# Kernel optimization log

Hardware: AMD Instinct MI355X
Metric: run time of the kernel (lower is better)

The kernel has to match this reference:

```python
import jax, jax.numpy as jnp
import numpy as np

EPS = 1e-7  # K.epsilon()
ITERATIONS = 5


def squash(v):
    # Faithful to the source: epsilon added elementwise to the vector first.
    v = v + EPS
    norm = jnp.sum(v * v, axis=-1, keepdims=True)  # squared norm
    scale = norm / (1.0 + norm) / jnp.sqrt(norm)
    return scale * v


def setup_inputs() -> dict:
    key = jax.random.key(0)
    k1, k2 = jax.random.split(key)
    B, I, D = 32, 2048, 16   # batch, input capsules, input capsule dim
    J, C = 64, 32            # output capsules, output capsule dim
    x = jax.random.normal(k1, (B, I, D), dtype=jnp.float32)
    # glorot_uniform for w_ij (fan_in = D, fan_out = C on the contracting dims)
    limit = np.sqrt(6.0 / (D + C)).astype(np.float32)
    w_ij = jax.random.uniform(k2, (J, I, C, D), dtype=jnp.float32,
                              minval=-limit, maxval=limit)
    return {"x": x, "w_ij": w_ij}


def reference(x, w_ij):
    # x: [B, I, D], w_ij: [J, I, C, D]
    # prediction vectors u_hat: [B, J, I, C]
    u_hat = jnp.einsum('bid,jicd->bjic', x, w_ij)
    B, J, I, C = u_hat.shape
    b_ij = jnp.zeros((B, J, I), dtype=u_hat.dtype)
    v_j = None
    for it in range(ITERATIONS):
        c_ij = jax.nn.softmax(b_ij, axis=1)          # softmax over output caps J
        s_j = jnp.einsum('bji,bjic->bjc', c_ij, u_hat)
        v_j = squash(s_j)                            # [B, J, C]
        if it < ITERATIONS - 1:
            b_ij = b_ij + jnp.einsum('bjc,bjic->bji', v_j, u_hat)
    return v_j
```

## Files before the change

kernel.cpp:

```cpp
#include <hip/hip_runtime.h>
#include <hip/hip_bf16.h>

#define B_ 32
#define I_ 2048
#define D_ 16
#define J_ 64
#define C_ 32

typedef float f32x16 __attribute__((ext_vector_type(16)));
typedef float f32x4a __attribute__((ext_vector_type(4)));
typedef short bf16x8 __attribute__((ext_vector_type(8)));

union BF8 { unsigned u[4]; bf16x8 v; };

__device__ __forceinline__ float bf2f(unsigned short u) {
  unsigned v = ((unsigned)u) << 16;
  float f;
  __builtin_memcpy(&f, &v, 4);
  return f;
}
__device__ __forceinline__ unsigned short f2bf(float f) {
  unsigned u;
  __builtin_memcpy(&u, &f, 4);
  u += 0x7FFFu + ((u >> 16) & 1u);
  return (unsigned short)(u >> 16);
}
__device__ __forceinline__ unsigned pk2(float lo, float hi) {
  return (unsigned)f2bf(lo) | ((unsigned)f2bf(hi) << 16);
}

__global__ __launch_bounds__(256) void prep_w(const float* __restrict__ w,
                                              unsigned short* __restrict__ w_bf,
                                              unsigned short* __restrict__ w2) {
  __shared__ float tr[16 * 33];
  const int tid = threadIdx.x;
  const int j = blockIdx.y, i0 = blockIdx.x * 16;
  for (int ii = 0; ii < 16; ++ii) {
    size_t base = ((size_t)j * I_ + i0 + ii) * 512;
    float2 v2 = *(const float2*)(w + base + 2 * tid);
    ((unsigned*)(w_bf + base))[tid] = pk2(v2.x, v2.y);
    int c = (2 * tid) >> 4, d = (2 * tid) & 15;
    tr[d * 33 + c] = v2.x;
    tr[(d + 1) * 33 + c] = v2.y;
    __syncthreads();
    int d2 = (2 * tid) >> 5, c2 = (2 * tid) & 31;
    ((unsigned*)(w2 + base))[tid] = pk2(tr[d2 * 33 + c2], tr[d2 * 33 + c2 + 1]);
    __syncthreads();
  }
}

__global__ __launch_bounds__(256) void prep_x4(const float* __restrict__ x,
                                               unsigned short* __restrict__ x4) {
  int g = blockIdx.x * 256 + threadIdx.x;
  int b = g & 31, o2 = (g >> 5) & 1, i = g >> 6;
  const float* xp = x + ((size_t)b * I_ + i) * D_ + o2 * 8;
  float4 a = *(const float4*)xp;
  float4 c = *(const float4*)(xp + 4);
  BF8 o;
  o.u[0] = pk2(a.x, a.y);
  o.u[1] = pk2(a.z, a.w);
  o.u[2] = pk2(c.x, c.y);
  o.u[3] = pk2(c.z, c.w);
  ((bf16x8*)x4)[g] = o.v;
}

template <int ACCUM, int WRITEB>
__global__ __launch_bounds__(256) void pass_bdot(const float* __restrict__ x,
                                                 const unsigned short* __restrict__ w2,
                                                 const float* __restrict__ vg,
                                                 float* __restrict__ b_run,
                                                 unsigned short* __restrict__ c_bf) {
  __shared__ float x_lds[32 * 36];
  __shared__ float bd[64 * 64];
  __shared__ unsigned short c_l[64 * 64];
  const int tid = threadIdx.x;
  const int i0 = blockIdx.x * 2;

  {
    int b = tid >> 3, idx = (tid & 7) * 4;
    int i_loc = idx >> 4, d = idx & 15;
    float4 v4 = *(const float4*)(x + ((size_t)b * I_ + i0 + i_loc) * D_ + d);
    *(float4*)(x_lds + b * 36 + idx) = v4;
  }
  __syncthreads();

  const int lane = tid & 63;
  const int wv = tid >> 6;
  const int ml = lane & 31;
  const int h = lane >> 5;

  f32x4a xr0 = *(const f32x4a*)(x_lds + ml * 36 + 4 * h);
  f32x4a xr1 = *(const f32x4a*)(x_lds + ml * 36 + 8 + 4 * h);
  f32x4a xr2 = *(const f32x4a*)(x_lds + ml * 36 + 16 + 4 * h);
  f32x4a xr3 = *(const f32x4a*)(x_lds + ml * 36 + 24 + 4 * h);

  for (int j = wv; j < 64; j += 4) {
    BF8 Bf0, Bf1, Af0, Af1;
    {
      const float* vp = vg + ((size_t)ml * J_ + j) * C_ + h * 8;
      float4 a = *(const float4*)vp;
      float4 b4 = *(const float4*)(vp + 4);
      Bf0.u[0] = pk2(a.x, a.y); Bf0.u[1] = pk2(a.z, a.w);
      Bf0.u[2] = pk2(b4.x, b4.y); Bf0.u[3] = pk2(b4.z, b4.w);
      const float* vp1 = vp + 16;
      float4 a1 = *(const float4*)vp1;
      float4 b5 = *(const float4*)(vp1 + 4);
      Bf1.u[0] = pk2(a1.x, a1.y); Bf1.u[1] = pk2(a1.z, a1.w);
      Bf1.u[2] = pk2(b5.x, b5.y); Bf1.u[3] = pk2(b5.z, b5.w);
    }
    {
      const unsigned short* wp =
          w2 + (((size_t)j * I_ + i0 + (ml >> 4)) * 16 + (ml & 15)) * 32 + h * 8;
      Af0.v = *(const bf16x8*)wp;
      Af1.v = *(const bf16x8*)(wp + 16);
    }
    f32x16 acc = 0.0f;
    acc = __builtin_amdgcn_mfma_f32_32x32x16_bf16(Af0.v, Bf0.v, acc, 0, 0, 0);
    acc = __builtin_amdgcn_mfma_f32_32x32x16_bf16(Af1.v, Bf1.v, acc, 0, 0, 0);
    float s0 = 0.f, s1 = 0.f;
#pragma unroll
    for (int r = 0; r < 4; ++r) s0 += acc[r] * xr0[r];
#pragma unroll
    for (int r = 0; r < 4; ++r) s0 += acc[4 + r] * xr1[r];
#pragma unroll
    for (int r = 0; r < 4; ++r) s1 += acc[8 + r] * xr2[r];
#pragma unroll
    for (int r = 0; r < 4; ++r) s1 += acc[12 + r] * xr3[r];
    s0 += __shfl_xor(s0, 32);
    s1 += __shfl_xor(s1, 32);
    bd[j * 64 + h * 32 + ml] = h ? s1 : s0;
  }
  __syncthreads();

  if (ACCUM) {
#pragma unroll 4
    for (int rep = 0; rep < 16; ++rep) {
      int idx = rep * 256 + tid;
      int j = idx >> 6, q = idx & 63, ii = q >> 5, b = q & 31;
      bd[idx] += b_run[((size_t)j * I_ + i0 + ii) * 32 + b];
    }
    __syncthreads();
  }
  if (WRITEB) {
#pragma unroll 4
    for (int rep = 0; rep < 16; ++rep) {
      int idx = rep * 256 + tid;
      int j = idx >> 6, q = idx & 63, ii = q >> 5, b = q & 31;
      b_run[((size_t)j * I_ + i0 + ii) * 32 + b] = bd[idx];
    }
  }
  __syncthreads();

  if (tid < 64) {
    int q = tid;
    float m = -1e30f;
    for (int j = 0; j < 64; ++j) m = fmaxf(m, bd[j * 64 + q]);
    float sum = 0.f;
    for (int j = 0; j < 64; ++j) {
      float e = __expf(bd[j * 64 + q] - m);
      bd[j * 64 + q] = e;
      sum += e;
    }
    float inv = 1.0f / sum;
    for (int j = 0; j < 64; ++j) c_l[j * 64 + q] = f2bf(bd[j * 64 + q] * inv);
  }
  __syncthreads();

#pragma unroll 4
  for (int rep = 0; rep < 8; ++rep) {
    int idx = rep * 256 + tid;
    int j = idx >> 5, q2 = idx & 31;
    unsigned val = (unsigned)c_l[j * 64 + 2 * q2] | ((unsigned)c_l[j * 64 + 2 * q2 + 1] << 16);
    *(unsigned*)(c_bf + ((size_t)j * I_ + i0) * 32 + 2 * q2) = val;
  }
}

template <int UNIFORM>
__global__ __launch_bounds__(256) void pass_s(const unsigned short* __restrict__ w_bf,
                                              const unsigned short* __restrict__ x4,
                                              const unsigned short* __restrict__ c_bf,
                                              float* __restrict__ gpart) {
  __shared__ float s_part[4][1024];
  const int tid = threadIdx.x, lane = tid & 63, wv = tid >> 6;
  const int j = blockIdx.y;
  const int slice = blockIdx.x;
  const int ibase = slice * 128 + wv * 32;
  const int ml = lane & 31, h = lane >> 5;
  f32x16 acc = 0.0f;
#pragma unroll 4
  for (int ii = 0; ii < 32; ++ii) {
    int i = ibase + ii;
    BF8 xa;
    xa.v = *(const bf16x8*)(x4 + (((size_t)i * 2 + h) * 32 + ml) * 8);
    float cf;
    if (UNIFORM) cf = 1.0f / 64.0f;
    else cf = bf2f(c_bf[((size_t)j * I_ + i) * 32 + ml]);
    BF8 ya;
#pragma unroll
    for (int p = 0; p < 4; ++p) {
      unsigned short lo16 = (unsigned short)(xa.u[p] & 0xFFFFu);
      unsigned short hi16 = (unsigned short)(xa.u[p] >> 16);
      ya.u[p] = pk2(bf2f(lo16) * cf, bf2f(hi16) * cf);
    }
    BF8 wb;
    wb.v = *(const bf16x8*)(w_bf + ((size_t)j * I_ + i) * 512 + ml * 16 + h * 8);
    acc = __builtin_amdgcn_mfma_f32_32x32x16_bf16(ya.v, wb.v, acc, 0, 0, 0);
  }
#pragma unroll
  for (int r = 0; r < 16; ++r) {
    int b = (r & 3) + 8 * (r >> 2) + 4 * h;
    s_part[wv][b * 32 + ml] = acc[r];
  }
  __syncthreads();
#pragma unroll
  for (int q = 0; q < 4; ++q) {
    int idx = q * 256 + tid;
    float t = s_part[0][idx] + s_part[1][idx] + s_part[2][idx] + s_part[3][idx];
    int b = idx >> 5, c = idx & 31;
    gpart[(((size_t)slice * B_ + b) * J_ + j) * C_ + c] = t;
  }
}

__global__ __launch_bounds__(256) void reduce_squash(const float* __restrict__ gpart,
                                                     float* __restrict__ vg,
                                                     float* __restrict__ outg,
                                                     int write_out) {
  const int gid = blockIdx.x * 256 + threadIdx.x;
  float sum = 0.f;
#pragma unroll
  for (int s = 0; s < 16; ++s) sum += gpart[(size_t)s * (B_ * J_ * C_) + gid];
  float t = sum + 1e-7f;
  float sq = t * t;
#pragma unroll
  for (int m = 16; m >= 1; m >>= 1) sq += __shfl_xor(sq, m);
  const float scale = sq / (1.0f + sq) / sqrtf(sq);
  vg[gid] = scale * t;
  if (write_out) outg[gid] = scale * t;
}

__global__ __launch_bounds__(256) void caps_squash(const float* __restrict__ sg,
                                                   float* __restrict__ vg,
                                                   float* __restrict__ outg,
                                                   int write_out) {
  const int r = blockIdx.x * blockDim.x + threadIdx.x;
  if (r >= B_ * J_) return;
  const float* sp = sg + (size_t)r * C_;
  float vals[C_];
  float norm = 0.f;
#pragma unroll
  for (int cc = 0; cc < C_; ++cc) {
    float t = sp[cc] + 1e-7f;
    vals[cc] = t;
    norm += t * t;
  }
  const float scale = norm / (1.0f + norm) / sqrtf(norm);
  float* vp = vg + (size_t)r * C_;
#pragma unroll
  for (int cc = 0; cc < C_; ++cc) vp[cc] = scale * vals[cc];
  if (write_out) {
    float* op = outg + (size_t)r * C_;
#pragma unroll
    for (int cc = 0; cc < C_; ++cc) op[cc] = scale * vals[cc];
  }
}

__device__ __forceinline__ float dot16(const float4* __restrict__ wp,
                                       float4 x0, float4 x1, float4 x2, float4 x3) {
  float4 a0 = wp[0], a1 = wp[1], a2 = wp[2], a3 = wp[3];
  float u = a0.x * x0.x + a0.y * x0.y + a0.z * x0.z + a0.w * x0.w;
  u += a1.x * x1.x + a1.y * x1.y + a1.z * x1.z + a1.w * x1.w;
  u += a2.x * x2.x + a2.y * x2.y + a2.z * x2.z + a2.w * x2.w;
  u += a3.x * x3.x + a3.y * x3.y + a3.z * x3.z + a3.w * x3.w;
  return u;
}

template <int UNIFORM, int READB, int WRITEB>
__global__ __launch_bounds__(256) void caps_pass(const float* __restrict__ x,
                                                 const float* __restrict__ w,
                                                 const float* __restrict__ vg,
                                                 float* __restrict__ bio,
                                                 float* __restrict__ sg) {
  __shared__ float s_acc[4][J_ * C_];
  const int tid = threadIdx.x;
  for (int idx = tid; idx < 4 * J_ * C_; idx += 256) ((float*)s_acc)[idx] = 0.f;
  __syncthreads();
  const int lane = tid & 63;
  const int wv = tid >> 6;
  const int b = blockIdx.y;
  const int h = lane >> 5;
  const int c = lane & 31;
  const int i0 = blockIdx.x * 64 + wv * 16;
  for (int ii = 0; ii < 16; ++ii) {
    const int i = i0 + ii;
    const float4* xp = (const float4*)(x + ((size_t)b * I_ + i) * D_);
    float4 x0 = xp[0], x1 = xp[1], x2 = xp[2], x3 = xp[3];
    float uk[32];
    float bk[32];
#pragma unroll
    for (int k = 0; k < 32; ++k) {
      const int j = 2 * k + h;
      const float4* wp = (const float4*)(w + (((size_t)j * I_ + i) * C_ + c) * D_);
      float u = dot16(wp, x0, x1, x2, x3);
      uk[k] = u;
      if (!UNIFORM) {
        float p = vg[(b * J_ + j) * C_ + c] * u;
        p += __shfl_xor(p, 16, 32);
        p += __shfl_xor(p, 8, 32);
        p += __shfl_xor(p, 4, 32);
        p += __shfl_xor(p, 2, 32);
        p += __shfl_xor(p, 1, 32);
        bk[k] = p;
      }
    }
    if (UNIFORM) {
#pragma unroll
      for (int k = 0; k < 32; ++k)
        s_acc[wv][(2 * k + h) * C_ + c] += uk[k] * (1.0f / (float)J_);
    } else {
      if (READB) {
        float breg = bio[((size_t)b * I_ + i) * J_ + lane];
#pragma unroll
        for (int k = 0; k < 32; ++k) bk[k] += __shfl(breg, 2 * k + h);
      }
      if (WRITEB) {
        float bsel = bk[0];
#pragma unroll
        for (int k = 1; k < 32; ++k) bsel = (c == k) ? bk[k] : bsel;
        bio[((size_t)b * I_ + i) * J_ + 2 * c + h] = bsel;
      }
      float m = bk[0];
#pragma unroll
      for (int k = 1; k < 32; ++k) m = fmaxf(m, bk[k]);
      m = fmaxf(m, __shfl_xor(m, 32));
      float sum = 0.f;
#pragma unroll
      for (int k = 0; k < 32; ++k) {
        bk[k] = __expf(bk[k] - m);
        sum += bk[k];
      }
      sum += __shfl_xor(sum, 32);
      const float inv = 1.0f / sum;
#pragma unroll
      for (int k = 0; k < 32; ++k)
        s_acc[wv][(2 * k + h) * C_ + c] += bk[k] * inv * uk[k];
    }
  }
  __syncthreads();
  for (int jc = tid; jc < J_ * C_; jc += 256) {
    float t = s_acc[0][jc] + s_acc[1][jc] + s_acc[2][jc] + s_acc[3][jc];
    atomicAdd(&sg[(size_t)b * J_ * C_ + jc], t);
  }
}

extern "C" void kernel_launch(void* const* d_in, const int* in_sizes, int n_in,
                              void* d_out, int out_size, void* d_ws, size_t ws_size,
                              hipStream_t stream) {
  const float* x = (const float*)d_in[0];
  const float* w = (const float*)d_in[1];
  float* out = (float*)d_out;

  const size_t SZ_WBF = (size_t)J_ * I_ * C_ * D_ * 2;
  const size_t SZ_W2 = SZ_WBF;
  const size_t SZ_X4 = (size_t)B_ * I_ * D_ * 2;
  const size_t SZ_CBF = (size_t)J_ * I_ * B_ * 2;
  const size_t SZ_BRUN = (size_t)J_ * I_ * B_ * 4;
  const size_t SZ_GP = (size_t)16 * B_ * J_ * C_ * 4;
  const size_t SZ_V = (size_t)B_ * J_ * C_ * 4;
  const size_t NEED = SZ_WBF + SZ_W2 + SZ_X4 + SZ_CBF + SZ_BRUN + SZ_GP + SZ_V;

  if (ws_size >= NEED) {
    char* p = (char*)d_ws;
    unsigned short* w_bf = (unsigned short*)p;  p += SZ_WBF;
    unsigned short* w2 = (unsigned short*)p;    p += SZ_W2;
    unsigned short* x4 = (unsigned short*)p;    p += SZ_X4;
    unsigned short* c_bf = (unsigned short*)p;  p += SZ_CBF;
    float* b_run = (float*)p;                   p += SZ_BRUN;
    float* gpart = (float*)p;                   p += SZ_GP;
    float* v_ws = (float*)p;

    prep_w<<<dim3(I_ / 16, J_), 256, 0, stream>>>(w, w_bf, w2);
    prep_x4<<<dim3((B_ * I_ * 2) / 256), 256, 0, stream>>>(x, x4);

    dim3 agrid(I_ / 2), bgrid(I_ / 128, J_), rgrid((B_ * J_ * C_) / 256);

    pass_s<1><<<bgrid, 256, 0, stream>>>(w_bf, x4, c_bf, gpart);
    reduce_squash<<<rgrid, 256, 0, stream>>>(gpart, v_ws, out, 0);
    pass_bdot<0, 1><<<agrid, 256, 0, stream>>>(x, w2, v_ws, b_run, c_bf);
    pass_s<0><<<bgrid, 256, 0, stream>>>(w_bf, x4, c_bf, gpart);
    reduce_squash<<<rgrid, 256, 0, stream>>>(gpart, v_ws, out, 0);
    pass_bdot<1, 1><<<agrid, 256, 0, stream>>>(x, w2, v_ws, b_run, c_bf);
    pass_s<0><<<bgrid, 256, 0, stream>>>(w_bf, x4, c_bf, gpart);
    reduce_squash<<<rgrid, 256, 0, stream>>>(gpart, v_ws, out, 0);
    pass_bdot<1, 1><<<agrid, 256, 0, stream>>>(x, w2, v_ws, b_run, c_bf);
    pass_s<0><<<bgrid, 256, 0, stream>>>(w_bf, x4, c_bf, gpart);
    reduce_squash<<<rgrid, 256, 0, stream>>>(gpart, v_ws, out, 0);
    pass_bdot<1, 0><<<agrid, 256, 0, stream>>>(x, w2, v_ws, b_run, c_bf);
    pass_s<0><<<bgrid, 256, 0, stream>>>(w_bf, x4, c_bf, gpart);
    reduce_squash<<<rgrid, 256, 0, stream>>>(gpart, v_ws, out, 1);
  } else {
    float* b_ws = (float*)d_ws;
    float* s_ws = b_ws + (size_t)B_ * I_ * J_;
    float* v_ws = s_ws + (size_t)B_ * J_ * C_;
    const size_t s_bytes = (size_t)B_ * J_ * C_ * sizeof(float);
    dim3 grid(I_ / 64, B_), blk(256);
    dim3 sgrid((B_ * J_ + 255) / 256), sblk(256);

    hipMemsetAsync(s_ws, 0, s_bytes, stream);
    caps_pass<1, 0, 0><<<grid, blk, 0, stream>>>(x, w, v_ws, b_ws, s_ws);
    caps_squash<<<sgrid, sblk, 0, stream>>>(s_ws, v_ws, out, 0);
    hipMemsetAsync(s_ws, 0, s_bytes, stream);
    caps_pass<0, 0, 1><<<grid, blk, 0, stream>>>(x, w, v_ws, b_ws, s_ws);
    caps_squash<<<sgrid, sblk, 0, stream>>>(s_ws, v_ws, out, 0);
    hipMemsetAsync(s_ws, 0, s_bytes, stream);
    caps_pass<0, 1, 1><<<grid, blk, 0, stream>>>(x, w, v_ws, b_ws, s_ws);
    caps_squash<<<sgrid, sblk, 0, stream>>>(s_ws, v_ws, out, 0);
    hipMemsetAsync(s_ws, 0, s_bytes, stream);
    caps_pass<0, 1, 1><<<grid, blk, 0, stream>>>(x, w, v_ws, b_ws, s_ws);
    caps_squash<<<sgrid, sblk, 0, stream>>>(s_ws, v_ws, out, 0);
    hipMemsetAsync(s_ws, 0, s_bytes, stream);
    caps_pass<0, 1, 0><<<grid, blk, 0, stream>>>(x, w, v_ws, b_ws, s_ws);
    caps_squash<<<sgrid, sblk, 0, stream>>>(s_ws, v_ws, out, 1);
  }
}
```

Baseline: 806.3 us.

## Batch loads ahead of MFMAs, store v as bf16, parallelize softmax, double pass_s grid

Replaces the software bf16 rounding with the hardware v_cvt_pk_bf16_f32 instruction. pass_bdot now issues eight W loads per batch before its MFMAs, reads a bf16 v written by reduce_squash instead of converting fp32 v per tile, and spreads the softmax over all four waves using cross-wave max and sum reductions. pass_s loads eight x, w and c values ahead of its MFMAs and covers half as many inputs per block, giving twice the blocks and twice the partials for reduce_squash to sum. The aim is more memory-level parallelism and less ALU conversion work, at the cost of more registers, extra barriers and a larger partial-sum buffer.

```diff
diff --git a/kernel.cpp b/kernel.cpp
--- a/kernel.cpp
+++ b/kernel.cpp
@@ -13,20 +13,22 @@
 
 union BF8 { unsigned u[4]; bf16x8 v; };
 
-__device__ __forceinline__ float bf2f(unsigned short u) {
-  unsigned v = ((unsigned)u) << 16;
+__device__ __forceinline__ unsigned cvtpk(float lo, float hi) {
+  unsigned r;
+  asm volatile("v_cvt_pk_bf16_f32 %0, %1, %2" : "=v"(r) : "v"(lo), "v"(hi));
+  return r;
+}
+__device__ __forceinline__ float asf(unsigned u) {
   float f;
-  __builtin_memcpy(&f, &v, 4);
+  __builtin_memcpy(&f, &u, 4);
   return f;
 }
+__device__ __forceinline__ float bf2f(unsigned short u) { return asf(((unsigned)u) << 16); }
 __device__ __forceinline__ unsigned short f2bf(float f) {
   unsigned u;
   __builtin_memcpy(&u, &f, 4);
   u += 0x7FFFu + ((u >> 16) & 1u);
   return (unsigned short)(u >> 16);
-}
-__device__ __forceinline__ unsigned pk2(float lo, float hi) {
-  return (unsigned)f2bf(lo) | ((unsigned)f2bf(hi) << 16);
 }
 
 __global__ __launch_bounds__(256) void prep_w(const float* __restrict__ w,
@@ -38,13 +40,13 @@
   for (int ii = 0; ii < 16; ++ii) {
     size_t base = ((size_t)j * I_ + i0 + ii) * 512;
     float2 v2 = *(const float2*)(w + base + 2 * tid);
-    ((unsigned*)(w_bf + base))[tid] = pk2(v2.x, v2.y);
+    ((unsigned*)(w_bf + base))[tid] = cvtpk(v2.x, v2.y);
     int c = (2 * tid) >> 4, d = (2 * tid) & 15;
     tr[d * 33 + c] = v2.x;
     tr[(d + 1) * 33 + c] = v2.y;
     __syncthreads();
     int d2 = (2 * tid) >> 5, c2 = (2 * tid) & 31;
-    ((unsigned*)(w2 + base))[tid] = pk2(tr[d2 * 33 + c2], tr[d2 * 33 + c2 + 1]);
+    ((unsigned*)(w2 + base))[tid] = cvtpk(tr[d2 * 33 + c2], tr[d2 * 33 + c2 + 1]);
     __syncthreads();
   }
 }
@@ -57,22 +59,23 @@
   float4 a = *(const float4*)xp;
   float4 c = *(const float4*)(xp + 4);
   BF8 o;
-  o.u[0] = pk2(a.x, a.y);
-  o.u[1] = pk2(a.z, a.w);
-  o.u[2] = pk2(c.x, c.y);
-  o.u[3] = pk2(c.z, c.w);
+  o.u[0] = cvtpk(a.x, a.y);
+  o.u[1] = cvtpk(a.z, a.w);
+  o.u[2] = cvtpk(c.x, c.y);
+  o.u[3] = cvtpk(c.z, c.w);
   ((bf16x8*)x4)[g] = o.v;
 }
 
 template <int ACCUM, int WRITEB>
 __global__ __launch_bounds__(256) void pass_bdot(const float* __restrict__ x,
                                                  const unsigned short* __restrict__ w2,
-                                                 const float* __restrict__ vg,
+                                                 const unsigned short* __restrict__ v_bf,
                                                  float* __restrict__ b_run,
                                                  unsigned short* __restrict__ c_bf) {
   __shared__ float x_lds[32 * 36];
   __shared__ float bd[64 * 64];
   __shared__ unsigned short c_l[64 * 64];
+  __shared__ float pm[4][64], ps[4][64];
   const int tid = threadIdx.x;
   const int i0 = blockIdx.x * 2;
 
@@ -94,41 +97,42 @@
   f32x4a xr2 = *(const f32x4a*)(x_lds + ml * 36 + 16 + 4 * h);
   f32x4a xr3 = *(const f32x4a*)(x_lds + ml * 36 + 24 + 4 * h);
 
-  for (int j = wv; j < 64; j += 4) {
-    BF8 Bf0, Bf1, Af0, Af1;
-    {
-      const float* vp = vg + ((size_t)ml * J_ + j) * C_ + h * 8;
-      float4 a = *(const float4*)vp;
-      float4 b4 = *(const float4*)(vp + 4);
-      Bf0.u[0] = pk2(a.x, a.y); Bf0.u[1] = pk2(a.z, a.w);
-      Bf0.u[2] = pk2(b4.x, b4.y); Bf0.u[3] = pk2(b4.z, b4.w);
-      const float* vp1 = vp + 16;
-      float4 a1 = *(const float4*)vp1;
-      float4 b5 = *(const float4*)(vp1 + 4);
-      Bf1.u[0] = pk2(a1.x, a1.y); Bf1.u[1] = pk2(a1.z, a1.w);
-      Bf1.u[2] = pk2(b5.x, b5.y); Bf1.u[3] = pk2(b5.z, b5.w);
-    }
-    {
-      const unsigned short* wp =
-          w2 + (((size_t)j * I_ + i0 + (ml >> 4)) * 16 + (ml & 15)) * 32 + h * 8;
-      Af0.v = *(const bf16x8*)wp;
-      Af1.v = *(const bf16x8*)(wp + 16);
-    }
-    f32x16 acc = 0.0f;
-    acc = __builtin_amdgcn_mfma_f32_32x32x16_bf16(Af0.v, Bf0.v, acc, 0, 0, 0);
-    acc = __builtin_amdgcn_mfma_f32_32x32x16_bf16(Af1.v, Bf1.v, acc, 0, 0, 0);
-    float s0 = 0.f, s1 = 0.f;
-#pragma unroll
-    for (int r = 0; r < 4; ++r) s0 += acc[r] * xr0[r];
-#pragma unroll
-    for (int r = 0; r < 4; ++r) s0 += acc[4 + r] * xr1[r];
-#pragma unroll
-    for (int r = 0; r < 4; ++r) s1 += acc[8 + r] * xr2[r];
-#pragma unroll
-    for (int r = 0; r < 4; ++r) s1 += acc[12 + r] * xr3[r];
-    s0 += __shfl_xor(s0, 32);
-    s1 += __shfl_xor(s1, 32);
-    bd[j * 64 + h * 32 + ml] = h ? s1 : s0;
+  const unsigned short* wbase = w2 + ((size_t)(i0 + (ml >> 4)) * 16 + (ml & 15)) * 32 + h * 8;
+  const unsigned short* vbase = v_bf + (size_t)ml * (J_ * C_) + h * 8;
+
+#pragma unroll
+  for (int half = 0; half < 2; ++half) {
+    BF8 Aw[8][2];
+#pragma unroll
+    for (int t = 0; t < 8; ++t) {
+      const int j = wv + (half * 8 + t) * 4;
+      const unsigned short* wp = wbase + (size_t)j * (I_ * 512);
+      Aw[t][0].v = *(const bf16x8*)wp;
+      Aw[t][1].v = *(const bf16x8*)(wp + 16);
+    }
+#pragma unroll
+    for (int t = 0; t < 8; ++t) {
+      const int j = wv + (half * 8 + t) * 4;
+      const unsigned short* vp = vbase + j * C_;
+      BF8 Bv0, Bv1;
+      Bv0.v = *(const bf16x8*)vp;
+      Bv1.v = *(const bf16x8*)(vp + 16);
+      f32x16 acc = 0.0f;
+      acc = __builtin_amdgcn_mfma_f32_32x32x16_bf16(Aw[t][0].v, Bv0.v, acc, 0, 0, 0);
+      acc = __builtin_amdgcn_mfma_f32_32x32x16_bf16(Aw[t][1].v, Bv1.v, acc, 0, 0, 0);
+      float s0 = 0.f, s1 = 0.f;
+#pragma unroll
+      for (int r = 0; r < 4; ++r) s0 += acc[r] * xr0[r];
+#pragma unroll
+      for (int r = 0; r < 4; ++r) s0 += acc[4 + r] * xr1[r];
+#pragma unroll
+      for (int r = 0; r < 4; ++r) s1 += acc[8 + r] * xr2[r];
+#pragma unroll
+      for (int r = 0; r < 4; ++r) s1 += acc[12 + r] * xr3[r];
+      s0 += __shfl_xor(s0, 32);
+      s1 += __shfl_xor(s1, 32);
+      bd[j * 64 + h * 32 + ml] = h ? s1 : s0;
+    }
   }
   __syncthreads();
 
@@ -148,21 +152,30 @@
       int j = idx >> 6, q = idx & 63, ii = q >> 5, b = q & 31;
       b_run[((size_t)j * I_ + i0 + ii) * 32 + b] = bd[idx];
     }
-  }
-  __syncthreads();
-
-  if (tid < 64) {
-    int q = tid;
+    __syncthreads();
+  }
+
+  {
+    const int q = tid & 63, part = tid >> 6;
+    const int jlo = part * 16;
     float m = -1e30f;
-    for (int j = 0; j < 64; ++j) m = fmaxf(m, bd[j * 64 + q]);
-    float sum = 0.f;
-    for (int j = 0; j < 64; ++j) {
-      float e = __expf(bd[j * 64 + q] - m);
-      bd[j * 64 + q] = e;
-      sum += e;
-    }
-    float inv = 1.0f / sum;
-    for (int j = 0; j < 64; ++j) c_l[j * 64 + q] = f2bf(bd[j * 64 + q] * inv);
+#pragma unroll
+    for (int jj = 0; jj < 16; ++jj) m = fmaxf(m, bd[(jlo + jj) * 64 + q]);
+    pm[part][q] = m;
+    __syncthreads();
+    const float M = fmaxf(fmaxf(pm[0][q], pm[1][q]), fmaxf(pm[2][q], pm[3][q]));
+    float s = 0.f;
+#pragma unroll
+    for (int jj = 0; jj < 16; ++jj) {
+      float e = __expf(bd[(jlo + jj) * 64 + q] - M);
+      bd[(jlo + jj) * 64 + q] = e;
+      s += e;
+    }
+    ps[part][q] = s;
+    __syncthreads();
+    const float inv = 1.0f / (ps[0][q] + ps[1][q] + ps[2][q] + ps[3][q]);
+#pragma unroll
+    for (int jj = 0; jj < 16; ++jj) c_l[(jlo + jj) * 64 + q] = f2bf(bd[(jlo + jj) * 64 + q] * inv);
   }
   __syncthreads();
 
@@ -184,28 +197,36 @@
   const int tid = threadIdx.x, lane = tid & 63, wv = tid >> 6;
   const int j = blockIdx.y;
   const int slice = blockIdx.x;
-  const int ibase = slice * 128 + wv * 32;
+  const int ibase = slice * 64 + wv * 16;
   const int ml = lane & 31, h = lane >> 5;
   f32x16 acc = 0.0f;
-#pragma unroll 4
-  for (int ii = 0; ii < 32; ++ii) {
-    int i = ibase + ii;
-    BF8 xa;
-    xa.v = *(const bf16x8*)(x4 + (((size_t)i * 2 + h) * 32 + ml) * 8);
-    float cf;
-    if (UNIFORM) cf = 1.0f / 64.0f;
-    else cf = bf2f(c_bf[((size_t)j * I_ + i) * 32 + ml]);
-    BF8 ya;
-#pragma unroll
-    for (int p = 0; p < 4; ++p) {
-      unsigned short lo16 = (unsigned short)(xa.u[p] & 0xFFFFu);
-      unsigned short hi16 = (unsigned short)(xa.u[p] >> 16);
-      ya.u[p] = pk2(bf2f(lo16) * cf, bf2f(hi16) * cf);
-    }
-    BF8 wb;
-    wb.v = *(const bf16x8*)(w_bf + ((size_t)j * I_ + i) * 512 + ml * 16 + h * 8);
-    acc = __builtin_amdgcn_mfma_f32_32x32x16_bf16(ya.v, wb.v, acc, 0, 0, 0);
-  }
+
+#pragma unroll
+  for (int half = 0; half < 2; ++half) {
+    const int i0 = ibase + half * 8;
+    BF8 xa[8], wb[8];
+    unsigned short cs[8];
+#pragma unroll
+    for (int t = 0; t < 8; ++t) {
+      const int i = i0 + t;
+      xa[t].v = *(const bf16x8*)(x4 + (((size_t)i * 2 + h) * 32 + ml) * 8);
+      wb[t].v = *(const bf16x8*)(w_bf + ((size_t)j * I_ + i) * 512 + ml * 16 + h * 8);
+      if (!UNIFORM) cs[t] = c_bf[((size_t)j * I_ + i) * 32 + ml];
+    }
+#pragma unroll
+    for (int t = 0; t < 8; ++t) {
+      const float cf = UNIFORM ? (1.0f / 64.0f) : bf2f(cs[t]);
+      BF8 ya;
+#pragma unroll
+      for (int p = 0; p < 4; ++p) {
+        float lo = asf(xa[t].u[p] << 16);
+        float hi = asf(xa[t].u[p] & 0xFFFF0000u);
+        ya.u[p] = cvtpk(lo * cf, hi * cf);
+      }
+      acc = __builtin_amdgcn_mfma_f32_32x32x16_bf16(ya.v, wb[t].v, acc, 0, 0, 0);
+    }
+  }
+
 #pragma unroll
   for (int r = 0; r < 16; ++r) {
     int b = (r & 3) + 8 * (r >> 2) + 4 * h;
@@ -222,20 +243,21 @@
 }
 
 __global__ __launch_bounds__(256) void reduce_squash(const float* __restrict__ gpart,
-                                                     float* __restrict__ vg,
+                                                     unsigned short* __restrict__ v_bf,
                                                      float* __restrict__ outg,
                                                      int write_out) {
   const int gid = blockIdx.x * 256 + threadIdx.x;
   float sum = 0.f;
 #pragma unroll
-  for (int s = 0; s < 16; ++s) sum += gpart[(size_t)s * (B_ * J_ * C_) + gid];
+  for (int s = 0; s < 32; ++s) sum += gpart[(size_t)s * (B_ * J_ * C_) + gid];
   float t = sum + 1e-7f;
   float sq = t * t;
 #pragma unroll
   for (int m = 16; m >= 1; m >>= 1) sq += __shfl_xor(sq, m);
   const float scale = sq / (1.0f + sq) / sqrtf(sq);
-  vg[gid] = scale * t;
-  if (write_out) outg[gid] = scale * t;
+  const float val = scale * t;
+  v_bf[gid] = f2bf(val);
+  if (write_out) outg[gid] = val;
 }
 
 __global__ __launch_bounds__(256) void caps_squash(const float* __restrict__ sg,
@@ -364,9 +386,9 @@
   const size_t SZ_X4 = (size_t)B_ * I_ * D_ * 2;
   const size_t SZ_CBF = (size_t)J_ * I_ * B_ * 2;
   const size_t SZ_BRUN = (size_t)J_ * I_ * B_ * 4;
-  const size_t SZ_GP = (size_t)16 * B_ * J_ * C_ * 4;
-  const size_t SZ_V = (size_t)B_ * J_ * C_ * 4;
-  const size_t NEED = SZ_WBF + SZ_W2 + SZ_X4 + SZ_CBF + SZ_BRUN + SZ_GP + SZ_V;
+  const size_t SZ_GP = (size_t)32 * B_ * J_ * C_ * 4;
+  const size_t SZ_VBF = (size_t)B_ * J_ * C_ * 2;
+  const size_t NEED = SZ_WBF + SZ_W2 + SZ_X4 + SZ_CBF + SZ_BRUN + SZ_GP + SZ_VBF;
 
   if (ws_size >= NEED) {
     char* p = (char*)d_ws;
@@ -376,27 +398,27 @@
     unsigned short* c_bf = (unsigned short*)p;  p += SZ_CBF;
     float* b_run = (float*)p;                   p += SZ_BRUN;
     float* gpart = (float*)p;                   p += SZ_GP;
-    float* v_ws = (float*)p;
+    unsigned short* v_bf = (unsigned short*)p;
 
     prep_w<<<dim3(I_ / 16, J_), 256, 0, stream>>>(w, w_bf, w2);
     prep_x4<<<dim3((B_ * I_ * 2) / 256), 256, 0, stream>>>(x, x4);
 
-    dim3 agrid(I_ / 2), bgrid(I_ / 128, J_), rgrid((B_ * J_ * C_) / 256);
+    dim3 agrid(I_ / 2), bgrid(32, J_), rgrid((B_ * J_ * C_) / 256);
 
     pass_s<1><<<bgrid, 256, 0, stream>>>(w_bf, x4, c_bf, gpart);
-    reduce_squash<<<rgrid, 256, 0, stream>>>(gpart, v_ws, out, 0);
-    pass_bdot<0, 1><<<agrid, 256, 0, stream>>>(x, w2, v_ws, b_run, c_bf);
+    reduce_squash<<<rgrid, 256, 0, stream>>>(gpart, v_bf, out, 0);
+    pass_bdot<0, 1><<<agrid, 256, 0, stream>>>(x, w2, v_bf, b_run, c_bf);
     pass_s<0><<<bgrid, 256, 0, stream>>>(w_bf, x4, c_bf, gpart);
-    reduce_squash<<<rgrid, 256, 0, stream>>>(gpart, v_ws, out, 0);
-    pass_bdot<1, 1><<<agrid, 256, 0, stream>>>(x, w2, v_ws, b_run, c_bf);
+    reduce_squash<<<rgrid, 256, 0, stream>>>(gpart, v_bf, out, 0);
+    pass_bdot<1, 1><<<agrid, 256, 0, stream>>>(x, w2, v_bf, b_run, c_bf);
     pass_s<0><<<bgrid, 256, 0, stream>>>(w_bf, x4, c_bf, gpart);
-    reduce_squash<<<rgrid, 256, 0, stream>>>(gpart, v_ws, out, 0);
-    pass_bdot<1, 1><<<agrid, 256, 0, stream>>>(x, w2, v_ws, b_run, c_bf);
+    reduce_squash<<<rgrid, 256, 0, stream>>>(gpart, v_bf, out, 0);
+    pass_bdot<1, 1><<<agrid, 256, 0, stream>>>(x, w2, v_bf, b_run, c_bf);
     pass_s<0><<<bgrid, 256, 0, stream>>>(w_bf, x4, c_bf, gpart);
-    reduce_squash<<<rgrid, 256, 0, stream>>>(gpart, v_ws, out, 0);
-    pass_bdot<1, 0><<<agrid, 256, 0, stream>>>(x, w2, v_ws, b_run, c_bf);
+    reduce_squash<<<rgrid, 256, 0, stream>>>(gpart, v_bf, out, 0);
+    pass_bdot<1, 0><<<agrid, 256, 0, stream>>>(x, w2, v_bf, b_run, c_bf);
     pass_s<0><<<bgrid, 256, 0, stream>>>(w_bf, x4, c_bf, gpart);
-    reduce_squash<<<rgrid, 256, 0, stream>>>(gpart, v_ws, out, 1);
+    reduce_squash<<<rgrid, 256, 0, stream>>>(gpart, v_bf, out, 1);
   } else {
     float* b_ws = (float*)d_ws;
     float* s_ws = b_ws + (size_t)B_ * I_ * J_;
```

Measured after the change: 730.0 us. 9.5% less time.
